# Optimization experiments

Measured on AMD Instinct MI355X. Metric: run time of the kernel, lower is better.

Reference implementation:

```python
import jax, jax.numpy as jnp
import numpy as np

B, NIN, NREG, D, H, L = 8, 1024, 16, 1024, 16, 12
DFF = 4 * D
S = NIN + NREG
HD = D // H
EPS = 1e-6


def setup_inputs() -> dict:
    key = jax.random.key(0)
    ks = jax.random.split(key, 8)
    p = lambda k, shape: jax.random.normal(k, shape, jnp.float32) * 0.02
    return dict(
        x=jax.random.normal(ks[0], (B, S, D), jnp.float32),
        n_input=NIN,
        ln1_g=jnp.ones((L, D), jnp.float32), ln1_b=jnp.zeros((L, D), jnp.float32),
        wqkv=p(ks[1], (L, D, 3 * D)), bqkv=jnp.zeros((L, 3 * D), jnp.float32),
        wo=p(ks[2], (L, D, D)), bo=jnp.zeros((L, D), jnp.float32),
        ln2_g=jnp.ones((L, D), jnp.float32), ln2_b=jnp.zeros((L, D), jnp.float32),
        w1=p(ks[3], (L, D, DFF)), b1=jnp.zeros((L, DFF), jnp.float32),
        w2=p(ks[4], (L, DFF, D)), b2=jnp.zeros((L, D), jnp.float32),
        lnf_g=jnp.ones((D,), jnp.float32), lnf_b=jnp.zeros((D,), jnp.float32),
    )


def _ln(x, g, b):
    mu = x.mean(-1, keepdims=True)
    var = ((x - mu) ** 2).mean(-1, keepdims=True)
    return (x - mu) * jax.lax.rsqrt(var + EPS) * g + b


def _build_mask(n_input, total):
    # inputs attend everywhere; registers attend to all inputs and causally among registers
    i = jnp.arange(total)[:, None]
    j = jnp.arange(total)[None, :]
    blocked = (i >= n_input) & (j >= n_input) & (j > i)
    return jnp.where(blocked, -jnp.inf, 0.0).astype(jnp.float32)  # (S, S) additive


def _attn(h, wqkv_l, bqkv_l, wo_l, bo_l, mask):
    b, s, _ = h.shape
    qkv = h @ wqkv_l + bqkv_l                                   # (B,S,3D)
    q, k, v = jnp.split(qkv, 3, axis=-1)
    q = q.reshape(b, s, H, HD).transpose(0, 2, 1, 3)            # (B,H,S,HD)
    k = k.reshape(b, s, H, HD).transpose(0, 2, 1, 3)
    v = v.reshape(b, s, H, HD).transpose(0, 2, 1, 3)
    scores = jnp.einsum('bhqd,bhkd->bhqk', q, k) / np.sqrt(HD) + mask
    a = jax.nn.softmax(scores, axis=-1)
    o = jnp.einsum('bhqk,bhkd->bhqd', a, v)
    o = o.transpose(0, 2, 1, 3).reshape(b, s, D)
    return o @ wo_l + bo_l


def reference(x, n_input, ln1_g, ln1_b, wqkv, bqkv, wo, bo,
              ln2_g, ln2_b, w1, b1, w2, b2, lnf_g, lnf_b):
    mask = _build_mask(n_input, x.shape[1])

    def blk(h, p):
        l1g, l1b, wq, bq, wo_, bo_, l2g, l2b, w1_, b1_, w2_, b2_ = p
        h = h + _attn(_ln(h, l1g, l1b), wq, bq, wo_, bo_, mask)
        u = _ln(h, l2g, l2b) @ w1_ + b1_
        h = h + jax.nn.gelu(u) @ w2_ + b2_
        return h, None

    h, _ = jax.lax.scan(blk, x, (ln1_g, ln1_b, wqkv, bqkv, wo, bo,
                                 ln2_g, ln2_b, w1, b1, w2, b2))
    return _ln(h, lnf_g, lnf_b)
```

## Files before the change

kernel.cpp:

```cpp
#include <hip/hip_runtime.h>
#include <hip/hip_bf16.h>
#include <stdint.h>

#define DD   1024
#define TD   3072
#define DFFN 4096
#define NL   12
#define SS   1040
#define SP   1056
#define BB   8
#define MM   (BB*SS)
#define HH   16
#define NTAIL 32

typedef float  f32x4  __attribute__((ext_vector_type(4)));
typedef __bf16 bf16x8 __attribute__((ext_vector_type(8)));
typedef unsigned short u16;

union Bf8 { bf16x8 v; u16 s[8]; };

__device__ __forceinline__ u16 f2b(float f) {
  union { float f; unsigned u; } x; x.f = f;
  unsigned r = (x.u + 0x7FFFu + ((x.u >> 16) & 1u)) >> 16;
  return (u16)r;
}

__device__ __forceinline__ f32x4 mfma_bf16(bf16x8 a, bf16x8 b, f32x4 c) {
  return __builtin_amdgcn_mfma_f32_16x16x32_bf16(a, b, c, 0, 0, 0);
}

__device__ __forceinline__ void gload_lds16(const u16* g, u16* l) {
  __builtin_amdgcn_global_load_lds((const __attribute__((address_space(1))) void*)g,
                                   (__attribute__((address_space(3))) void*)l, 16, 0, 0);
}

__device__ __forceinline__ float dppmax16(float t) {
  union { float f; int i; } u, v;
  u.f = t;
  v.i = __builtin_amdgcn_update_dpp(0, u.i, 0xB1, 0xF, 0xF, true);
  u.f = fmaxf(u.f, v.f);
  v.i = __builtin_amdgcn_update_dpp(0, u.i, 0x4E, 0xF, 0xF, true);
  u.f = fmaxf(u.f, v.f);
  v.i = __builtin_amdgcn_update_dpp(0, u.i, 0x124, 0xF, 0xF, true);
  u.f = fmaxf(u.f, v.f);
  v.i = __builtin_amdgcn_update_dpp(0, u.i, 0x128, 0xF, 0xF, true);
  u.f = fmaxf(u.f, v.f);
  return u.f;
}

__global__ __launch_bounds__(256)
void transpose_cast(const float* __restrict__ in, u16* __restrict__ out, int K, int N) {
  __shared__ float tile[32][33];
  const int n0 = blockIdx.x * 32, k0 = blockIdx.y * 32;
  const size_t lb = (size_t)blockIdx.z * K * N;
  const int tx = threadIdx.x, ty = threadIdx.y;
  for (int j = 0; j < 4; ++j)
    tile[ty + 8*j][tx] = in[lb + (size_t)(k0 + ty + 8*j) * N + n0 + tx];
  __syncthreads();
  for (int j = 0; j < 4; ++j)
    out[lb + (size_t)(n0 + ty + 8*j) * K + k0 + tx] = f2b(tile[tx][ty + 8*j]);
}

template<int OUTF>
__global__ __launch_bounds__(256)
void ln_kernel(const float* __restrict__ in, const float* __restrict__ gam,
               const float* __restrict__ bet, u16* __restrict__ outb, float* __restrict__ outf) {
  const int row = blockIdx.x, t = threadIdx.x;
  const float4 v = ((const float4*)(in + (size_t)row * DD))[t];
  float s  = v.x + v.y + v.z + v.w;
  float s2 = v.x*v.x + v.y*v.y + v.z*v.z + v.w*v.w;
  for (int off = 1; off < 64; off <<= 1) { s += __shfl_xor(s, off); s2 += __shfl_xor(s2, off); }
  __shared__ float red[8];
  if ((t & 63) == 0) { red[t >> 6] = s; red[4 + (t >> 6)] = s2; }
  __syncthreads();
  s  = red[0] + red[1] + red[2] + red[3];
  s2 = red[4] + red[5] + red[6] + red[7];
  const float mu = s * (1.0f/1024.0f);
  const float var = s2 * (1.0f/1024.0f) - mu*mu;
  const float rs = rsqrtf(var + 1e-6f);
  const float4 gv = ((const float4*)gam)[t];
  const float4 bv = ((const float4*)bet)[t];
  const float y0 = (v.x - mu)*rs*gv.x + bv.x;
  const float y1 = (v.y - mu)*rs*gv.y + bv.y;
  const float y2 = (v.z - mu)*rs*gv.z + bv.z;
  const float y3 = (v.w - mu)*rs*gv.w + bv.w;
  if (OUTF) {
    float4 o; o.x=y0; o.y=y1; o.z=y2; o.w=y3;
    ((float4*)(outf + (size_t)row * DD))[t] = o;
  } else {
    ushort4 o; o.x=f2b(y0); o.y=f2b(y1); o.z=f2b(y2); o.w=f2b(y3);
    ((ushort4*)(outb + (size_t)row * DD))[t] = o;
  }
}

template<int EPI>
__global__ __launch_bounds__(256, 4)
void gemm_bt(const u16* __restrict__ A, const u16* __restrict__ Bt,
             const float* __restrict__ bias, const float* __restrict__ resid,
             float* outF, u16* outB,
             u16* __restrict__ qb, u16* __restrict__ kb, u16* __restrict__ vtb,
             int N, int K) {
  __shared__ u16 As[128*64];
  __shared__ u16 Bs[128*64];
  const int tid = threadIdx.x;

  const int nwg = gridDim.x * gridDim.y;
  int wgid = blockIdx.y * gridDim.x + blockIdx.x;
  wgid = (wgid & 7) * (nwg >> 3) + (wgid >> 3);
  const int nb = wgid % gridDim.y;
  const int mb = wgid / gridDim.y;
  const int m0 = mb * 128, n0 = nb * 128;

  const int lane = tid & 63, w = tid >> 6;
  const int wr = (w >> 1) * 64, wc = (w & 1) * 64;
  const int c = lane & 15, g = lane >> 4;

  f32x4 acc[4][4];
  for (int i = 0; i < 4; ++i) for (int j = 0; j < 4; ++j) acc[i][j] = f32x4{0.f,0.f,0.f,0.f};

  const int srow = tid >> 3, scg = tid & 7;
  const size_t aoff = (size_t)(m0 + srow) * K + scg * 8;
  const size_t boff = (size_t)(n0 + srow) * K + scg * 8;

  for (int kt = 0; kt < K; kt += 64) {
    for (int it = 0; it < 4; ++it) {
      gload_lds16(A  + aoff + (size_t)it * 32 * K + kt, As + (it*256 + tid) * 8);
      gload_lds16(Bt + boff + (size_t)it * 32 * K + kt, Bs + (it*256 + tid) * 8);
    }
    __syncthreads();
    for (int kk = 0; kk < 2; ++kk) {
      bf16x8 af[4], bfr[4];
      for (int i = 0; i < 4; ++i) af[i]  = *(const bf16x8*)(As + (wr + i*16 + c)*64 + kk*32 + g*8);
      for (int j = 0; j < 4; ++j) bfr[j] = *(const bf16x8*)(Bs + (wc + j*16 + c)*64 + kk*32 + g*8);
      for (int i = 0; i < 4; ++i)
        for (int j = 0; j < 4; ++j)
          acc[i][j] = mfma_bf16(af[i], bfr[j], acc[i][j]);
    }
    __syncthreads();
  }

  for (int j = 0; j < 4; ++j) {
    const int col = n0 + wc + j*16 + c;
    const float bcol = bias[col];
    for (int i = 0; i < 4; ++i) {
      const int row0 = m0 + wr + i*16 + 4*g;
      if (EPI == 3) {
        const int part = col >> 10;
        const int hh2  = (col >> 6) & 15;
        const int hd   = col & 63;
        const int bb   = (int)((unsigned)row0 / SS);
        const int s0   = row0 - bb * SS;
        const size_t bh = (size_t)(bb * HH + hh2);
        if (part == 2) {
          ushort4 pk;
          pk.x = f2b(acc[i][j][0] + bcol);
          pk.y = f2b(acc[i][j][1] + bcol);
          pk.z = f2b(acc[i][j][2] + bcol);
          pk.w = f2b(acc[i][j][3] + bcol);
          *(ushort4*)(vtb + (bh*64 + hd)*SP + s0) = pk;
        } else if (part == 0) {
          for (int r = 0; r < 4; ++r)
            qb[(bh*SP + s0 + r)*64 + hd] = f2b((acc[i][j][r] + bcol) * 0.125f);
        } else {
          for (int r = 0; r < 4; ++r)
            kb[(bh*SP + s0 + r)*64 + hd] = f2b(acc[i][j][r] + bcol);
        }
      } else {
        for (int r = 0; r < 4; ++r) {
          const size_t idx = (size_t)(row0 + r) * N + col;
          const float v = acc[i][j][r] + bcol;
          if (EPI == 1) {
            const float z = 1.5957691216f * (v + 0.044715f * v * v * v);
            const float e = __expf(z);
            outB[idx] = f2b(v * e * __builtin_amdgcn_rcpf(e + 1.0f));
          } else {
            outF[idx] = v + resid[idx];
          }
        }
      }
    }
  }
}

__global__ __launch_bounds__(512, 2)
void gemm_splitk(const u16* __restrict__ A, const u16* __restrict__ Bt,
                 const float* __restrict__ bias, const float* __restrict__ resid,
                 float* __restrict__ outF, int N, int K) {
  __shared__ u16 smem[4 * 128 * 64];
  const int tid = threadIdx.x;
  const int gg = tid >> 8;
  const int t2 = tid & 255;

  u16* As = smem + gg * (128*64);
  u16* Bs = smem + 2*(128*64) + gg * (128*64);

  const int nwg = gridDim.x * gridDim.y;
  int wgid = blockIdx.y * gridDim.x + blockIdx.x;
  wgid = (wgid & 7) * (nwg >> 3) + (wgid >> 3);
  const int nb = wgid % gridDim.y;
  const int mb = wgid / gridDim.y;
  const int m0 = mb * 128, n0 = nb * 128;

  const int lane = tid & 63, w = (tid >> 6) & 3;
  const int wr = (w >> 1) * 64, wc = (w & 1) * 64;
  const int c = lane & 15, g = lane >> 4;

  f32x4 acc[4][4];
  for (int i = 0; i < 4; ++i) for (int j = 0; j < 4; ++j) acc[i][j] = f32x4{0.f,0.f,0.f,0.f};

  const int srow = t2 >> 3, scg = t2 & 7;
  const int kbase = gg * (K >> 1);
  const size_t aoff = (size_t)(m0 + srow) * K + scg * 8 + kbase;
  const size_t boff = (size_t)(n0 + srow) * K + scg * 8 + kbase;

  const int KH = K >> 1;
  for (int kt = 0; kt < KH; kt += 64) {
    for (int it = 0; it < 4; ++it) {
      gload_lds16(A  + aoff + (size_t)it * 32 * K + kt, As + (it*256 + t2) * 8);
      gload_lds16(Bt + boff + (size_t)it * 32 * K + kt, Bs + (it*256 + t2) * 8);
    }
    __syncthreads();
    for (int kk = 0; kk < 2; ++kk) {
      bf16x8 af[4], bfr[4];
      for (int i = 0; i < 4; ++i) af[i]  = *(const bf16x8*)(As + (wr + i*16 + c)*64 + kk*32 + g*8);
      for (int j = 0; j < 4; ++j) bfr[j] = *(const bf16x8*)(Bs + (wc + j*16 + c)*64 + kk*32 + g*8);
      for (int i = 0; i < 4; ++i)
        for (int j = 0; j < 4; ++j)
          acc[i][j] = mfma_bf16(af[i], bfr[j], acc[i][j]);
    }
    __syncthreads();
  }

  f32x4* Red = (f32x4*)smem;
  if (gg == 1) {
#pragma unroll
    for (int k = 0; k < 16; ++k)
      Red[k * 256 + t2] = acc[k >> 2][k & 3];
  }
  __syncthreads();
  if (gg == 0) {
#pragma unroll
    for (int k = 0; k < 16; ++k) {
      const f32x4 v = Red[k * 256 + t2];
      acc[k >> 2][k & 3] += v;
    }
    for (int j = 0; j < 4; ++j) {
      const int col = n0 + wc + j*16 + c;
      const float bcol = bias[col];
      for (int i = 0; i < 4; ++i) {
        const int row0 = m0 + wr + i*16 + 4*g;
        for (int r = 0; r < 4; ++r) {
          const size_t idx = (size_t)(row0 + r) * N + col;
          outF[idx] = acc[i][j][r] + bcol + resid[idx];
        }
      }
    }
  }
}

__global__ __launch_bounds__(256, 4)
void gemm64(const u16* __restrict__ A, const u16* __restrict__ Bt,
            const float* __restrict__ bias, const float* __restrict__ resid,
            float* __restrict__ outF, int N, int K) {
  __shared__ u16 As[64*64];
  __shared__ u16 Bs[128*64];
  const int tid = threadIdx.x;

  const int nwg = gridDim.x * gridDim.y;
  int wgid = blockIdx.y * gridDim.x + blockIdx.x;
  wgid = (wgid & 7) * (nwg >> 3) + (wgid >> 3);
  const int nb = wgid % gridDim.y;
  const int mb = wgid / gridDim.y;
  const int m0 = mb * 64, n0 = nb * 128;

  const int lane = tid & 63, w = tid >> 6;
  const int wr = (w >> 1) * 32, wc = (w & 1) * 64;
  const int c = lane & 15, g = lane >> 4;

  f32x4 acc[2][4];
  for (int i = 0; i < 2; ++i) for (int j = 0; j < 4; ++j) acc[i][j] = f32x4{0.f,0.f,0.f,0.f};

  const int srow = tid >> 3, scg = tid & 7;
  const size_t aoff = (size_t)(m0 + srow) * K + scg * 8;
  const size_t boff = (size_t)(n0 + srow) * K + scg * 8;

  for (int kt = 0; kt < K; kt += 64) {
    for (int it = 0; it < 2; ++it)
      gload_lds16(A  + aoff + (size_t)it * 32 * K + kt, As + (it*256 + tid) * 8);
    for (int it = 0; it < 4; ++it)
      gload_lds16(Bt + boff + (size_t)it * 32 * K + kt, Bs + (it*256 + tid) * 8);
    __syncthreads();
    for (int kk = 0; kk < 2; ++kk) {
      bf16x8 af[2], bfr[4];
      for (int i = 0; i < 2; ++i) af[i]  = *(const bf16x8*)(As + (wr + i*16 + c)*64 + kk*32 + g*8);
      for (int j = 0; j < 4; ++j) bfr[j] = *(const bf16x8*)(Bs + (wc + j*16 + c)*64 + kk*32 + g*8);
      for (int i = 0; i < 2; ++i)
        for (int j = 0; j < 4; ++j)
          acc[i][j] = mfma_bf16(af[i], bfr[j], acc[i][j]);
    }
    __syncthreads();
  }

  for (int j = 0; j < 4; ++j) {
    const int col = n0 + wc + j*16 + c;
    const float bcol = bias[col];
    for (int i = 0; i < 2; ++i) {
      const int row0 = m0 + wr + i*16 + 4*g;
      for (int r = 0; r < 4; ++r) {
        const size_t idx = (size_t)(row0 + r) * N + col;
        outF[idx] = acc[i][j][r] + bcol + resid[idx];
      }
    }
  }
}

__global__ __launch_bounds__(256, 4)
void attn_staged(const u16* __restrict__ Qb, const u16* __restrict__ Kb,
                 const u16* __restrict__ VTb, u16* __restrict__ out,
                 const int* __restrict__ npt) {
  __shared__ u16 KV[2][4096];
  __shared__ u16 PT[4][640];
  const int tid = threadIdx.x;
  const int w = tid >> 6, lane = tid & 63;
  const int c = lane & 15, g = lane >> 4;
  const int nin = npt[0];
  u16* pw = PT[w];

  if (blockIdx.x < NTAIL) {
    const int bh = blockIdx.x * 4 + w;
    const int b = bh >> 4, hh = bh & 15;
    const int q0 = 64 * 16;

    bf16x8 aq0, aq1;
    {
      const u16* qp = Qb + ((size_t)bh * SP + q0 + c) * 64 + g * 8;
      aq0 = *(const bf16x8*)qp;
      aq1 = *(const bf16x8*)(qp + 32);
    }

    float m[4], ls[4];
    f32x4 o[4];
    int qrow[4];
    for (int r = 0; r < 4; ++r) { m[r] = -1e30f; ls[r] = 0.f; qrow[r] = q0 + 4*g + r; }
    for (int nd = 0; nd < 4; ++nd) o[nd] = f32x4{0.f,0.f,0.f,0.f};

    for (int kt = 0; kt < 33; ++kt) {
      const int k0 = kt * 32;

      f32x4 s[2];
      {
        const u16* kp0 = Kb + ((size_t)bh * SP + k0 + c) * 64 + g * 8;
        f32x4 z0 = f32x4{0.f,0.f,0.f,0.f};
        z0 = mfma_bf16(aq0, *(const bf16x8*)kp0, z0);
        z0 = mfma_bf16(aq1, *(const bf16x8*)(kp0 + 32), z0);
        s[0] = z0;
        const u16* kp1 = kp0 + 16 * 64;
        f32x4 z1 = f32x4{0.f,0.f,0.f,0.f};
        z1 = mfma_bf16(aq0, *(const bf16x8*)kp1, z1);
        z1 = mfma_bf16(aq1, *(const bf16x8*)(kp1 + 32), z1);
        s[1] = z1;
      }

      for (int jt = 0; jt < 2; ++jt) {
        const int j = k0 + jt*16 + c;
        for (int r = 0; r < 4; ++r) {
          const int q = qrow[r];
          const bool blocked = (j >= SS) || ((q >= nin) && (j >= nin) && (j > q));
          if (blocked) s[jt][r] = -1e30f;
        }
      }

      for (int r = 0; r < 4; ++r) {
        float t = fmaxf(s[0][r], s[1][r]);
        for (int off = 1; off < 16; off <<= 1) t = fmaxf(t, __shfl_xor(t, off));
        const float mn = fmaxf(m[r], t);
        const float al = __expf(m[r] - mn);
        m[r] = mn;
        const float p0 = __expf(s[0][r] - mn);
        const float p1 = __expf(s[1][r] - mn);
        s[0][r] = p0; s[1][r] = p1;
        float ps = p0 + p1;
        for (int off = 1; off < 16; off <<= 1) ps += __shfl_xor(ps, off);
        ls[r] = ls[r] * al + ps;
        for (int nd = 0; nd < 4; ++nd) o[nd][r] *= al;
      }

      for (int jt = 0; jt < 2; ++jt)
        for (int r = 0; r < 4; ++r)
          pw[(4*g + r)*40 + jt*16 + c] = f2b(s[jt][r]);
      __builtin_amdgcn_sched_barrier(0);
      bf16x8 ap = *(const bf16x8*)(pw + c*40 + 8*g);
      __builtin_amdgcn_sched_barrier(0);

      for (int nd = 0; nd < 4; ++nd) {
        const u16* vp = VTb + ((size_t)bh * 64 + nd*16 + c) * SP + k0 + 8*g;
        o[nd] = mfma_bf16(ap, *(const bf16x8*)vp, o[nd]);
      }
    }

    for (int nd = 0; nd < 4; ++nd)
      for (int r = 0; r < 4; ++r) {
        const float v = o[nd][r] / ls[r];
        out[((size_t)b * SS + qrow[r]) * DD + hh*64 + nd*16 + c] = f2b(v);
      }
    return;
  }

  const int sb = blockIdx.x - NTAIL;
  const int bh = sb & 127;
  const int qg = sb >> 7;
  const int b = bh >> 4, hh = bh & 15;

  const u16 *ssrc0, *ssrc1; int kstr; u16 *sdst0, *sdst1;
  if (tid < 128) {
    const int i0 = tid, i1 = tid + 128;
    const int r0 = i0 >> 3, cg0 = (i0 & 7) ^ (r0 & 7);
    const int r1 = i1 >> 3, cg1 = (i1 & 7) ^ (r1 & 7);
    ssrc0 = Kb + ((size_t)bh * SP + r0) * 64 + cg0 * 8;
    ssrc1 = Kb + ((size_t)bh * SP + r1) * 64 + cg1 * 8;
    kstr = 32 * 64;
    sdst0 = &KV[0][i0 * 8];
    sdst1 = &KV[0][i1 * 8];
  } else {
    const int t2 = tid - 128;
    const int i0 = t2, i1 = t2 + 128;
    const int r0 = i0 >> 2, cg0 = (i0 & 3) ^ (r0 & 3);
    const int r1 = i1 >> 2, cg1 = (i1 & 3) ^ (r1 & 3);
    ssrc0 = VTb + ((size_t)bh * 64 + r0) * SP + cg0 * 8;
    ssrc1 = VTb + ((size_t)bh * 64 + r1) * SP + cg1 * 8;
    kstr = 32;
    sdst0 = &KV[0][2048 + i0 * 8];
    sdst1 = &KV[0][2048 + i1 * 8];
  }
#define STAGE(bufbit, kt) do { \
    gload_lds16(ssrc0 + (size_t)(kt) * kstr, sdst0 + (bufbit) * 4096); \
    gload_lds16(ssrc1 + (size_t)(kt) * kstr, sdst1 + (bufbit) * 4096); } while (0)

  bf16x8 aq[2][2];
  int q0[2];
#pragma unroll
  for (int qq = 0; qq < 2; ++qq) {
    q0[qq] = (qg * 8 + w * 2 + qq) * 16;
    const u16* qp = Qb + ((size_t)bh * SP + q0[qq] + c) * 64 + g * 8;
    aq[qq][0] = *(const bf16x8*)qp;
    aq[qq][1] = *(const bf16x8*)(qp + 32);
  }

  Bf8 onesf;
  for (int i = 0; i < 8; ++i) onesf.s[i] = (c == 0) ? (u16)0x3F80 : (u16)0;

  float m[2][4];
  f32x4 o[2][5];
#pragma unroll
  for (int qq = 0; qq < 2; ++qq) {
    for (int r = 0; r < 4; ++r) m[qq][r] = -1e30f;
    for (int nd = 0; nd < 5; ++nd) o[qq][nd] = f32x4{0.f,0.f,0.f,0.f};
  }
  const bool tregs0 = (q0[0] + 15) >= nin;
  const bool tregs1 = (q0[1] + 15) >= nin;
  const int c7 = c & 7, c3 = c & 3;

  STAGE(0, 0);

  for (int kt = 0; kt < 33; ++kt) {
    const int buf = kt & 1;
    __syncthreads();
    if (kt < 32) STAGE(buf ^ 1, kt + 1);
    const u16* Kt = &KV[buf][0];
    const u16* Vt = &KV[buf][2048];
    const int k0 = kt * 32;

    bf16x8 k00 = *(const bf16x8*)(Kt + c*64        + ((g    ) ^ c7) * 8);
    bf16x8 k01 = *(const bf16x8*)(Kt + c*64        + ((g + 4) ^ c7) * 8);
    bf16x8 k10 = *(const bf16x8*)(Kt + (c+16)*64   + ((g    ) ^ c7) * 8);
    bf16x8 k11 = *(const bf16x8*)(Kt + (c+16)*64   + ((g + 4) ^ c7) * 8);

#pragma unroll
    for (int qq = 0; qq < 2; ++qq) {
      f32x4 s[2];
      {
        f32x4 z0 = f32x4{0.f,0.f,0.f,0.f};
        z0 = mfma_bf16(aq[qq][0], k00, z0);
        z0 = mfma_bf16(aq[qq][1], k01, z0);
        s[0] = z0;
        f32x4 z1 = f32x4{0.f,0.f,0.f,0.f};
        z1 = mfma_bf16(aq[qq][0], k10, z1);
        z1 = mfma_bf16(aq[qq][1], k11, z1);
        s[1] = z1;
      }

      const bool tregs = qq ? tregs1 : tregs0;
      if (tregs || (k0 + 31 >= SS)) {
        const int qr0 = q0[qq] + 4*g;
        for (int jt = 0; jt < 2; ++jt) {
          const int j = k0 + jt*16 + c;
          for (int r = 0; r < 4; ++r) {
            const int q = qr0 + r;
            const bool blocked = (j >= SS) || ((q >= nin) && (j >= nin) && (j > q));
            if (blocked) s[jt][r] = -1e30f;
          }
        }
      }

      for (int r = 0; r < 4; ++r) {
        const float t = dppmax16(fmaxf(s[0][r], s[1][r]));
        const float mn = fmaxf(m[qq][r], t);
        const float al = __expf(m[qq][r] - mn);
        m[qq][r] = mn;
        for (int nd = 0; nd < 5; ++nd) o[qq][nd][r] *= al;
        s[0][r] = __expf(s[0][r] - mn);
        s[1][r] = __expf(s[1][r] - mn);
      }

      for (int jt = 0; jt < 2; ++jt)
        for (int r = 0; r < 4; ++r)
          pw[(4*g + r)*40 + jt*16 + c] = f2b(s[jt][r]);
      __builtin_amdgcn_sched_barrier(0);
      bf16x8 ap = *(const bf16x8*)(pw + c*40 + 8*g);
      __builtin_amdgcn_sched_barrier(0);

      for (int nd = 0; nd < 4; ++nd) {
        bf16x8 bv = *(const bf16x8*)(Vt + (nd*16 + c)*32 + ((g ^ c3) * 8));
        o[qq][nd] = mfma_bf16(ap, bv, o[qq][nd]);
      }
      o[qq][4] = mfma_bf16(ap, onesf.v, o[qq][4]);
    }
  }
#undef STAGE

#pragma unroll
  for (int qq = 0; qq < 2; ++qq) {
    float rls[4];
    for (int r = 0; r < 4; ++r)
      rls[r] = 1.0f / __shfl(o[qq][4][r], lane & 48);
    const int qr0 = q0[qq] + 4*g;
    for (int nd = 0; nd < 4; ++nd)
      for (int r = 0; r < 4; ++r)
        out[((size_t)b * SS + qr0 + r) * DD + hh*64 + nd*16 + c] = f2b(o[qq][nd][r] * rls[r]);
  }
}

extern "C" void kernel_launch(void* const* d_in, const int* in_sizes, int n_in,
                              void* d_out, int out_size, void* d_ws, size_t ws_size,
                              hipStream_t stream) {
  const float* x    = (const float*)d_in[0];
  const int*   npt  = (const int*)  d_in[1];
  const float* ln1g = (const float*)d_in[2];
  const float* ln1b = (const float*)d_in[3];
  const float* wqkv = (const float*)d_in[4];
  const float* bqkv = (const float*)d_in[5];
  const float* wo   = (const float*)d_in[6];
  const float* bo   = (const float*)d_in[7];
  const float* ln2g = (const float*)d_in[8];
  const float* ln2b = (const float*)d_in[9];
  const float* w1   = (const float*)d_in[10];
  const float* b1   = (const float*)d_in[11];
  const float* w2   = (const float*)d_in[12];
  const float* b2   = (const float*)d_in[13];
  const float* lnfg = (const float*)d_in[14];
  const float* lnfb = (const float*)d_in[15];

  char* ws = (char*)d_ws;
  size_t off = 0;
  u16*   wqkvT = (u16*)(ws + off);   off += (size_t)NL*TD*DD*2;
  u16*   woT   = (u16*)(ws + off);   off += (size_t)NL*DD*DD*2;
  u16*   w1T   = (u16*)(ws + off);   off += (size_t)NL*DFFN*DD*2;
  u16*   w2T   = (u16*)(ws + off);   off += (size_t)NL*DD*DFFN*2;
  float* h     = (float*)(ws + off); off += (size_t)MM*DD*4;
  u16*   lnb   = (u16*)(ws + off);   off += (size_t)MM*DD*2;
  u16*   Qb    = (u16*)(ws + off);   off += (size_t)BB*HH*SP*64*2;
  u16*   Kb    = (u16*)(ws + off);   off += (size_t)BB*HH*SP*64*2;
  u16*   VTb   = (u16*)(ws + off);   off += (size_t)BB*HH*64*SP*2;
  u16*   attnO = (u16*)(ws + off);   off += (size_t)MM*DD*2;
  u16*   ffh   = (u16*)(ws + off);   off += (size_t)MM*DFFN*2;

  const dim3 tb(32, 8);
  transpose_cast<<<dim3(TD/32,   DD/32,   NL), tb, 0, stream>>>(wqkv, wqkvT, DD,   TD);
  transpose_cast<<<dim3(DD/32,   DD/32,   NL), tb, 0, stream>>>(wo,   woT,   DD,   DD);
  transpose_cast<<<dim3(DFFN/32, DD/32,   NL), tb, 0, stream>>>(w1,   w1T,   DD,   DFFN);
  transpose_cast<<<dim3(DD/32,   DFFN/32, NL), tb, 0, stream>>>(w2,   w2T,   DFFN, DD);
  hipMemcpyAsync(h, x, (size_t)MM*DD*4, hipMemcpyDeviceToDevice, stream);
  hipMemsetAsync(Qb, 0, (size_t)3*BB*HH*SP*64*2, stream);

  for (int l = 0; l < NL; ++l) {
    ln_kernel<0><<<MM, 256, 0, stream>>>(h, ln1g + (size_t)l*DD, ln1b + (size_t)l*DD, lnb, nullptr);
    gemm_bt<3><<<dim3(MM/128, TD/128), 256, 0, stream>>>(
        lnb, wqkvT + (size_t)l*TD*DD, bqkv + (size_t)l*TD, nullptr, nullptr, nullptr,
        Qb, Kb, VTb, TD, DD);
    attn_staged<<<dim3(1024 + NTAIL), 256, 0, stream>>>(Qb, Kb, VTb, attnO, npt);
    gemm64<<<dim3(MM/64, DD/128), 256, 0, stream>>>(
        attnO, woT + (size_t)l*DD*DD, bo + (size_t)l*DD, h, h, DD, DD);
    ln_kernel<0><<<MM, 256, 0, stream>>>(h, ln2g + (size_t)l*DD, ln2b + (size_t)l*DD, lnb, nullptr);
    gemm_bt<1><<<dim3(MM/128, DFFN/128), 256, 0, stream>>>(
        lnb, w1T + (size_t)l*DFFN*DD, b1 + (size_t)l*DFFN, nullptr, nullptr, ffh,
        nullptr, nullptr, nullptr, DFFN, DD);
    gemm_splitk<<<dim3(MM/128, DD/128), 512, 0, stream>>>(
        ffh, w2T + (size_t)l*DD*DFFN, b2 + (size_t)l*DD, h, h, DD, DFFN);
  }
  ln_kernel<1><<<MM, 256, 0, stream>>>(h, lnfg, lnfb, nullptr, (float*)d_out);
}
```

Baseline: 6.729 ms.

## Split FFN2 K-halves across blocks and fuse partial-sum reduction into next LayerNorm

```diff
diff --git a/kernel.cpp b/kernel.cpp
--- a/kernel.cpp
+++ b/kernel.cpp
@@ -61,12 +61,43 @@
     out[lb + (size_t)(n0 + ty + 8*j) * K + k0 + tx] = f2b(tile[tx][ty + 8*j]);
 }
 
+__global__ __launch_bounds__(256)
+void ln_kernel(const float* __restrict__ in, const float* __restrict__ gam,
+               const float* __restrict__ bet, u16* __restrict__ outb) {
+  const int row = blockIdx.x, t = threadIdx.x;
+  const float4 v = ((const float4*)(in + (size_t)row * DD))[t];
+  float s  = v.x + v.y + v.z + v.w;
+  float s2 = v.x*v.x + v.y*v.y + v.z*v.z + v.w*v.w;
+  for (int off = 1; off < 64; off <<= 1) { s += __shfl_xor(s, off); s2 += __shfl_xor(s2, off); }
+  __shared__ float red[8];
+  if ((t & 63) == 0) { red[t >> 6] = s; red[4 + (t >> 6)] = s2; }
+  __syncthreads();
+  s  = red[0] + red[1] + red[2] + red[3];
+  s2 = red[4] + red[5] + red[6] + red[7];
+  const float mu = s * (1.0f/1024.0f);
+  const float var = s2 * (1.0f/1024.0f) - mu*mu;
+  const float rs = rsqrtf(var + 1e-6f);
+  const float4 gv = ((const float4*)gam)[t];
+  const float4 bv = ((const float4*)bet)[t];
+  ushort4 o;
+  o.x = f2b((v.x - mu)*rs*gv.x + bv.x);
+  o.y = f2b((v.y - mu)*rs*gv.y + bv.y);
+  o.z = f2b((v.z - mu)*rs*gv.z + bv.z);
+  o.w = f2b((v.w - mu)*rs*gv.w + bv.w);
+  ((ushort4*)(outb + (size_t)row * DD))[t] = o;
+}
+
 template<int OUTF>
 __global__ __launch_bounds__(256)
-void ln_kernel(const float* __restrict__ in, const float* __restrict__ gam,
-               const float* __restrict__ bet, u16* __restrict__ outb, float* __restrict__ outf) {
+void ln_comb(const float* __restrict__ P0, const float* __restrict__ P1,
+             float* __restrict__ hout, const float* __restrict__ gam,
+             const float* __restrict__ bet, u16* __restrict__ outb,
+             float* __restrict__ outf) {
   const int row = blockIdx.x, t = threadIdx.x;
-  const float4 v = ((const float4*)(in + (size_t)row * DD))[t];
+  const float4 a = ((const float4*)(P0 + (size_t)row * DD))[t];
+  const float4 b = ((const float4*)(P1 + (size_t)row * DD))[t];
+  float4 v; v.x = a.x + b.x; v.y = a.y + b.y; v.z = a.z + b.z; v.w = a.w + b.w;
+  ((float4*)(hout + (size_t)row * DD))[t] = v;
   float s  = v.x + v.y + v.z + v.w;
   float s2 = v.x*v.x + v.y*v.y + v.z*v.z + v.w*v.w;
   for (int off = 1; off < 64; off <<= 1) { s += __shfl_xor(s, off); s2 += __shfl_xor(s2, off); }
@@ -182,17 +213,14 @@
   }
 }
 
-__global__ __launch_bounds__(512, 2)
-void gemm_splitk(const u16* __restrict__ A, const u16* __restrict__ Bt,
-                 const float* __restrict__ bias, const float* __restrict__ resid,
-                 float* __restrict__ outF, int N, int K) {
-  __shared__ u16 smem[4 * 128 * 64];
+__global__ __launch_bounds__(256, 4)
+void gemm_ffn2(const u16* __restrict__ A, const u16* __restrict__ Bt,
+               const float* __restrict__ bias, const float* __restrict__ resid,
+               float* __restrict__ P0, float* __restrict__ P1, int N, int K) {
+  __shared__ u16 As[128*64];
+  __shared__ u16 Bs[128*64];
   const int tid = threadIdx.x;
-  const int gg = tid >> 8;
-  const int t2 = tid & 255;
-
-  u16* As = smem + gg * (128*64);
-  u16* Bs = smem + 2*(128*64) + gg * (128*64);
+  const int kh = blockIdx.z;
 
   const int nwg = gridDim.x * gridDim.y;
   int wgid = blockIdx.y * gridDim.x + blockIdx.x;
@@ -201,23 +229,22 @@
   const int mb = wgid / gridDim.y;
   const int m0 = mb * 128, n0 = nb * 128;
 
-  const int lane = tid & 63, w = (tid >> 6) & 3;
+  const int lane = tid & 63, w = tid >> 6;
   const int wr = (w >> 1) * 64, wc = (w & 1) * 64;
   const int c = lane & 15, g = lane >> 4;
 
   f32x4 acc[4][4];
   for (int i = 0; i < 4; ++i) for (int j = 0; j < 4; ++j) acc[i][j] = f32x4{0.f,0.f,0.f,0.f};
 
-  const int srow = t2 >> 3, scg = t2 & 7;
-  const int kbase = gg * (K >> 1);
-  const size_t aoff = (size_t)(m0 + srow) * K + scg * 8 + kbase;
-  const size_t boff = (size_t)(n0 + srow) * K + scg * 8 + kbase;
-
   const int KH = K >> 1;
+  const int srow = tid >> 3, scg = tid & 7;
+  const size_t aoff = (size_t)(m0 + srow) * K + scg * 8 + (size_t)kh * KH;
+  const size_t boff = (size_t)(n0 + srow) * K + scg * 8 + (size_t)kh * KH;
+
   for (int kt = 0; kt < KH; kt += 64) {
     for (int it = 0; it < 4; ++it) {
-      gload_lds16(A  + aoff + (size_t)it * 32 * K + kt, As + (it*256 + t2) * 8);
-      gload_lds16(Bt + boff + (size_t)it * 32 * K + kt, Bs + (it*256 + t2) * 8);
+      gload_lds16(A  + aoff + (size_t)it * 32 * K + kt, As + (it*256 + tid) * 8);
+      gload_lds16(Bt + boff + (size_t)it * 32 * K + kt, Bs + (it*256 + tid) * 8);
     }
     __syncthreads();
     for (int kk = 0; kk < 2; ++kk) {
@@ -231,28 +258,17 @@
     __syncthreads();
   }
 
-  f32x4* Red = (f32x4*)smem;
-  if (gg == 1) {
-#pragma unroll
-    for (int k = 0; k < 16; ++k)
-      Red[k * 256 + t2] = acc[k >> 2][k & 3];
-  }
-  __syncthreads();
-  if (gg == 0) {
-#pragma unroll
-    for (int k = 0; k < 16; ++k) {
-      const f32x4 v = Red[k * 256 + t2];
-      acc[k >> 2][k & 3] += v;
-    }
-    for (int j = 0; j < 4; ++j) {
-      const int col = n0 + wc + j*16 + c;
-      const float bcol = bias[col];
-      for (int i = 0; i < 4; ++i) {
-        const int row0 = m0 + wr + i*16 + 4*g;
-        for (int r = 0; r < 4; ++r) {
-          const size_t idx = (size_t)(row0 + r) * N + col;
-          outF[idx] = acc[i][j][r] + bcol + resid[idx];
-        }
+  float* outP = kh ? P1 : P0;
+  for (int j = 0; j < 4; ++j) {
+    const int col = n0 + wc + j*16 + c;
+    const float bcol = kh ? 0.f : bias[col];
+    for (int i = 0; i < 4; ++i) {
+      const int row0 = m0 + wr + i*16 + 4*g;
+      for (int r = 0; r < 4; ++r) {
+        const size_t idx = (size_t)(row0 + r) * N + col;
+        float v = acc[i][j][r] + bcol;
+        if (!kh) v += resid[idx];
+        outP[idx] = v;
       }
     }
   }
@@ -573,6 +589,8 @@
   u16*   VTb   = (u16*)(ws + off);   off += (size_t)BB*HH*64*SP*2;
   u16*   attnO = (u16*)(ws + off);   off += (size_t)MM*DD*2;
   u16*   ffh   = (u16*)(ws + off);   off += (size_t)MM*DFFN*2;
+  float* P0    = (float*)(ws + off); off += (size_t)MM*DD*4;
+  float* P1    = (float*)(ws + off); off += (size_t)MM*DD*4;
 
   const dim3 tb(32, 8);
   transpose_cast<<<dim3(TD/32,   DD/32,   NL), tb, 0, stream>>>(wqkv, wqkvT, DD,   TD);
@@ -583,19 +601,23 @@
   hipMemsetAsync(Qb, 0, (size_t)3*BB*HH*SP*64*2, stream);
 
   for (int l = 0; l < NL; ++l) {
-    ln_kernel<0><<<MM, 256, 0, stream>>>(h, ln1g + (size_t)l*DD, ln1b + (size_t)l*DD, lnb, nullptr);
+    if (l == 0)
+      ln_kernel<<<MM, 256, 0, stream>>>(h, ln1g, ln1b, lnb);
+    else
+      ln_comb<0><<<MM, 256, 0, stream>>>(P0, P1, h, ln1g + (size_t)l*DD, ln1b + (size_t)l*DD,
+                                         lnb, nullptr);
     gemm_bt<3><<<dim3(MM/128, TD/128), 256, 0, stream>>>(
         lnb, wqkvT + (size_t)l*TD*DD, bqkv + (size_t)l*TD, nullptr, nullptr, nullptr,
         Qb, Kb, VTb, TD, DD);
     attn_staged<<<dim3(1024 + NTAIL), 256, 0, stream>>>(Qb, Kb, VTb, attnO, npt);
     gemm64<<<dim3(MM/64, DD/128), 256, 0, stream>>>(
         attnO, woT + (size_t)l*DD*DD, bo + (size_t)l*DD, h, h, DD, DD);
-    ln_kernel<0><<<MM, 256, 0, stream>>>(h, ln2g + (size_t)l*DD, ln2b + (size_t)l*DD, lnb, nullptr);
+    ln_kernel<<<MM, 256, 0, stream>>>(h, ln2g + (size_t)l*DD, ln2b + (size_t)l*DD, lnb);
     gemm_bt<1><<<dim3(MM/128, DFFN/128), 256, 0, stream>>>(
         lnb, w1T + (size_t)l*DFFN*DD, b1 + (size_t)l*DFFN, nullptr, nullptr, ffh,
         nullptr, nullptr, nullptr, DFFN, DD);
-    gemm_splitk<<<dim3(MM/128, DD/128), 512, 0, stream>>>(
-        ffh, w2T + (size_t)l*DD*DFFN, b2 + (size_t)l*DD, h, h, DD, DFFN);
-  }
-  ln_kernel<1><<<MM, 256, 0, stream>>>(h, lnfg, lnfb, nullptr, (float*)d_out);
-}
+    gemm_ffn2<<<dim3(MM/128, DD/128, 2), 256, 0, stream>>>(
+        ffh, w2T + (size_t)l*DD*DFFN, b2 + (size_t)l*DD, h, P0, P1, DD, DFFN);
+  }
+  ln_comb<1><<<MM, 256, 0, stream>>>(P0, P1, h, lnfg, lnfb, nullptr, (float*)d_out);
+}
```

Result: faster. 5.712 ms (median of 2 runs) (-15.1%).
